# Kernel optimization log

Hardware: AMD Instinct MI355X
Metric: run time of the kernel (lower is better)

Reference implementation:

```python
import jax, jax.numpy as jnp
import numpy as np

S, K, O = 8192, 1024, 4096  # seq_len, in_features, out_features


def setup_inputs() -> dict:
    key = jax.random.key(0)
    k1, k2, k3, k4, k5 = jax.random.split(key, 5)
    x = jax.random.randint(k1, (S, K), -128, 128, dtype=jnp.int8)
    weight_q = jax.random.randint(k2, (O, K), -128, 128, dtype=jnp.int8)
    scale_x = jax.random.uniform(k3, (), jnp.float32, 0.01, 0.1)
    scale_w = jax.random.uniform(k4, (), jnp.float32, 0.01, 0.1)
    scale_y = jax.random.uniform(k5, (S,), jnp.float32, 0.5, 2.0)  # per-row output scale
    return {"x": x, "weight_q": weight_q, "scale_x": scale_x,
            "scale_w": scale_w, "scale_y": scale_y}


def reference(x, weight_q, scale_x, scale_w, scale_y):
    # int8 GEMM with int32 accumulation: [S,K] @ [O,K]^T -> [S,O]
    acc = jnp.einsum('sk,ok->so', x.astype(jnp.int32), weight_q.astype(jnp.int32))
    # fused per-row requantization: scale_y[:seq_len] gives per-row scale
    requant_scale = (scale_x * scale_w / scale_y).astype(jnp.float32)  # [S]
    scaled = acc.astype(jnp.float32) * requant_scale[:, None]
    out_q = jnp.clip(jnp.round(scaled), -128.0, 127.0).astype(jnp.int8)
    return out_q, scale_y
```

## Files before the change

### kernel.cpp

```cpp
#include <hip/hip_runtime.h>


#define S_DIM 8192
#define K_DIM 1024
#define O_DIM 4096
#define BM 128
#define BN 128
#define BK 64
#define NITER (K_DIM / BK)
#define TILE_BYTES (BM * BK)

using i32x4 = __attribute__((ext_vector_type(4))) int;

__device__ __forceinline__ void load_lds16(const void* g, void* l) {
  __builtin_amdgcn_global_load_lds(
      (const __attribute__((address_space(1))) void*)g,
      (__attribute__((address_space(3))) void*)l, 16, 0, 0);
}

__global__ void pack_kernel(const int* __restrict__ xi, const int* __restrict__ wi,
                            const float* __restrict__ sy,
                            uint4* __restrict__ ap, uint4* __restrict__ bp,
                            float* __restrict__ out_sy) {
  const int tid = blockIdx.x * blockDim.x + threadIdx.x;
  const int nA = S_DIM * K_DIM / 16;
  const int nB = O_DIM * K_DIM / 16;

  const int4* s4 = nullptr;
  uint4* dst = nullptr;
  int j = 0;
  if (tid < nA) {
    j = tid;
    const int t = j >> 9, idx = j & 511;
    const int sub = idx >> 6, q = (idx >> 4) & 3, fr = idx & 15;
    const int band = t >> 4, kt = t & 15;
    const int row = band * 128 + sub * 16 + fr;
    s4 = (const int4*)xi + row * 256 + kt * 16 + q * 4;
    dst = ap;
  } else if (tid < nA + nB) {
    j = tid - nA;
    const int t = j >> 9, idx = j & 511;
    const int r = idx >> 2, cs = idx & 3, c = cs ^ (r & 3);
    const int band = t >> 4, kt = t & 15;
    const int row = band * 128 + r;
    s4 = (const int4*)wi + row * 256 + kt * 16 + c * 4;
    dst = bp;
  }
  if (s4) {
    int4 v0 = s4[0], v1 = s4[1], v2 = s4[2], v3 = s4[3];
    uint4 o;
    o.x = (v0.x & 0xff) | ((v0.y & 0xff) << 8) | ((v0.z & 0xff) << 16) | (((unsigned)v0.w & 0xff) << 24);
    o.y = (v1.x & 0xff) | ((v1.y & 0xff) << 8) | ((v1.z & 0xff) << 16) | (((unsigned)v1.w & 0xff) << 24);
    o.z = (v2.x & 0xff) | ((v2.y & 0xff) << 8) | ((v2.z & 0xff) << 16) | (((unsigned)v2.w & 0xff) << 24);
    o.w = (v3.x & 0xff) | ((v3.y & 0xff) << 8) | ((v3.z & 0xff) << 16) | (((unsigned)v3.w & 0xff) << 24);
    dst[j] = o;
  }
  if (tid < S_DIM) out_sy[tid] = sy[tid];
}

__global__ __launch_bounds__(256, 4) void gemm_i8_kernel(
    const signed char* __restrict__ Ap,
    const signed char* __restrict__ Bp,
    const float* __restrict__ sx, const float* __restrict__ sw,
    const float* __restrict__ sy, float* __restrict__ out) {
  __shared__ __align__(16) signed char Bs[2][TILE_BYTES];

  const int tid = threadIdx.x;
  const int wave = tid >> 6;
  const int lane = tid & 63;
  const int wm = wave >> 1;
  const int wn = wave & 1;
  const int rowBase = blockIdx.x * BM;
  const int colBase = blockIdx.y * BN;

  const int soff = wave * 1024 + lane * 16;
  const signed char* gB = Bp + (size_t)blockIdx.y * NITER * TILE_BYTES + soff;
  signed char* ldsB = (signed char*)Bs + wave * 1024;

  const signed char* gA = Ap + (size_t)blockIdx.x * NITER * TILE_BYTES +
                          wm * 4096 + lane * 16;

  i32x4 acc[4][4] = {};

  const int fr = lane & 15;
  const int fq = (((lane >> 4) ^ (fr & 3)) & 3) * 16;

  load_lds16(gB, ldsB);
  load_lds16(gB + 4096, ldsB + 4096);
  i32x4 af[2][4];
#pragma unroll
  for (int mi = 0; mi < 4; ++mi)
    af[0][mi] = *(const i32x4*)(gA + mi * 1024);

  for (int it = 0; it < NITER; ++it) {
    const int p = it & 1;
    __syncthreads();

    if (it + 1 < NITER) {
      const int boff = ((it + 1) & 1) * TILE_BYTES;
      const size_t goff = (size_t)(it + 1) * TILE_BYTES;
      load_lds16(gB + goff, ldsB + boff);
      load_lds16(gB + goff + 4096, ldsB + boff + 4096);
#pragma unroll
      for (int mi = 0; mi < 4; ++mi)
        af[p ^ 1][mi] = *(const i32x4*)(gA + goff + mi * 1024);
    }

    const signed char* curB = Bs[it & 1];
#pragma unroll
    for (int ni = 0; ni < 4; ++ni) {
      i32x4 bf = *(const i32x4*)(curB + (wn * 64 + ni * 16 + fr) * BK + fq);
#pragma unroll
      for (int mi = 0; mi < 4; ++mi)
        acc[mi][ni] =
            __builtin_amdgcn_mfma_i32_16x16x64_i8(af[p][mi], bf, acc[mi][ni], 0, 0, 0);
    }
  }

  const float sxw = sx[0] * sw[0];
  const int quad = lane >> 4;
#pragma unroll
  for (int mi = 0; mi < 4; ++mi) {
#pragma unroll
    for (int r = 0; r < 4; ++r) {
      const int s = rowBase + wm * 64 + mi * 16 + quad * 4 + r;
      const float rs = sxw / sy[s];
      float* orow = out + (size_t)s * O_DIM + colBase + wn * 64 + fr;
#pragma unroll
      for (int ni = 0; ni < 4; ++ni) {
        float f = rintf((float)acc[mi][ni][r] * rs);
        f = fminf(127.0f, fmaxf(-128.0f, f));
        orow[ni * 16] = f;
      }
    }
  }
}

extern "C" void kernel_launch(void* const* d_in, const int* in_sizes, int n_in,
                              void* d_out, int out_size, void* d_ws, size_t ws_size,
                              hipStream_t stream) {
  const int* x = (const int*)d_in[0];
  const int* w = (const int*)d_in[1];
  const float* sx = (const float*)d_in[2];
  const float* sw = (const float*)d_in[3];
  const float* sy = (const float*)d_in[4];
  float* out = (float*)d_out;

  uint4* ap = (uint4*)d_ws;
  uint4* bp = ap + (size_t)S_DIM * K_DIM / 16;

  const int total = S_DIM * K_DIM / 16 + O_DIM * K_DIM / 16;
  pack_kernel<<<(total + 255) / 256, 256, 0, stream>>>(
      x, w, sy, ap, bp, out + (size_t)S_DIM * O_DIM);

  dim3 grid(S_DIM / BM, O_DIM / BN);
  gemm_i8_kernel<<<grid, 256, 0, stream>>>(
      (const signed char*)ap, (const signed char*)bp, sx, sw, sy, out);
}
```

Before: 201.1 us.

## Load B fragments directly from global into registers, dropping LDS and barriers

Result: no change. 204.5 us (+1.7%).

```diff
diff --git a/kernel.cpp b/kernel.cpp
--- a/kernel.cpp
+++ b/kernel.cpp
@@ -12,12 +12,6 @@
 
 using i32x4 = __attribute__((ext_vector_type(4))) int;
 
-__device__ __forceinline__ void load_lds16(const void* g, void* l) {
-  __builtin_amdgcn_global_load_lds(
-      (const __attribute__((address_space(1))) void*)g,
-      (__attribute__((address_space(3))) void*)l, 16, 0, 0);
-}
-
 __global__ void pack_kernel(const int* __restrict__ xi, const int* __restrict__ wi,
                             const float* __restrict__ sy,
                             uint4* __restrict__ ap, uint4* __restrict__ bp,
@@ -26,27 +20,20 @@
   const int nA = S_DIM * K_DIM / 16;
   const int nB = O_DIM * K_DIM / 16;
 
-  const int4* s4 = nullptr;
+  const int4* src = nullptr;
   uint4* dst = nullptr;
   int j = 0;
   if (tid < nA) {
-    j = tid;
+    j = tid; src = (const int4*)xi; dst = ap;
+  } else if (tid < nA + nB) {
+    j = tid - nA; src = (const int4*)wi; dst = bp;
+  }
+  if (dst) {
     const int t = j >> 9, idx = j & 511;
     const int sub = idx >> 6, q = (idx >> 4) & 3, fr = idx & 15;
     const int band = t >> 4, kt = t & 15;
     const int row = band * 128 + sub * 16 + fr;
-    s4 = (const int4*)xi + row * 256 + kt * 16 + q * 4;
-    dst = ap;
-  } else if (tid < nA + nB) {
-    j = tid - nA;
-    const int t = j >> 9, idx = j & 511;
-    const int r = idx >> 2, cs = idx & 3, c = cs ^ (r & 3);
-    const int band = t >> 4, kt = t & 15;
-    const int row = band * 128 + r;
-    s4 = (const int4*)wi + row * 256 + kt * 16 + c * 4;
-    dst = bp;
-  }
-  if (s4) {
+    const int4* s4 = src + row * 256 + kt * 16 + q * 4;
     int4 v0 = s4[0], v1 = s4[1], v2 = s4[2], v3 = s4[3];
     uint4 o;
     o.x = (v0.x & 0xff) | ((v0.y & 0xff) << 8) | ((v0.z & 0xff) << 16) | (((unsigned)v0.w & 0xff) << 24);
@@ -58,13 +45,11 @@
   if (tid < S_DIM) out_sy[tid] = sy[tid];
 }
 
-__global__ __launch_bounds__(256, 4) void gemm_i8_kernel(
+__global__ __launch_bounds__(256, 3) void gemm_i8_kernel(
     const signed char* __restrict__ Ap,
     const signed char* __restrict__ Bp,
     const float* __restrict__ sx, const float* __restrict__ sw,
     const float* __restrict__ sy, float* __restrict__ out) {
-  __shared__ __align__(16) signed char Bs[2][TILE_BYTES];
-
   const int tid = threadIdx.x;
   const int wave = tid >> 6;
   const int lane = tid & 63;
@@ -73,51 +58,41 @@
   const int rowBase = blockIdx.x * BM;
   const int colBase = blockIdx.y * BN;
 
-  const int soff = wave * 1024 + lane * 16;
-  const signed char* gB = Bp + (size_t)blockIdx.y * NITER * TILE_BYTES + soff;
-  signed char* ldsB = (signed char*)Bs + wave * 1024;
-
   const signed char* gA = Ap + (size_t)blockIdx.x * NITER * TILE_BYTES +
                           wm * 4096 + lane * 16;
+  const signed char* gB = Bp + (size_t)blockIdx.y * NITER * TILE_BYTES +
+                          wn * 4096 + lane * 16;
 
   i32x4 acc[4][4] = {};
+  i32x4 af[2][4], bf[2][4];
 
-  const int fr = lane & 15;
-  const int fq = (((lane >> 4) ^ (fr & 3)) & 3) * 16;
+#pragma unroll
+  for (int mi = 0; mi < 4; ++mi) {
+    af[0][mi] = *(const i32x4*)(gA + mi * 1024);
+    bf[0][mi] = *(const i32x4*)(gB + mi * 1024);
+  }
 
-  load_lds16(gB, ldsB);
-  load_lds16(gB + 4096, ldsB + 4096);
-  i32x4 af[2][4];
-#pragma unroll
-  for (int mi = 0; mi < 4; ++mi)
-    af[0][mi] = *(const i32x4*)(gA + mi * 1024);
-
+#pragma unroll 2
   for (int it = 0; it < NITER; ++it) {
     const int p = it & 1;
-    __syncthreads();
-
     if (it + 1 < NITER) {
-      const int boff = ((it + 1) & 1) * TILE_BYTES;
       const size_t goff = (size_t)(it + 1) * TILE_BYTES;
-      load_lds16(gB + goff, ldsB + boff);
-      load_lds16(gB + goff + 4096, ldsB + boff + 4096);
 #pragma unroll
-      for (int mi = 0; mi < 4; ++mi)
+      for (int mi = 0; mi < 4; ++mi) {
         af[p ^ 1][mi] = *(const i32x4*)(gA + goff + mi * 1024);
+        bf[p ^ 1][mi] = *(const i32x4*)(gB + goff + mi * 1024);
+      }
     }
-
-    const signed char* curB = Bs[it & 1];
 #pragma unroll
-    for (int ni = 0; ni < 4; ++ni) {
-      i32x4 bf = *(const i32x4*)(curB + (wn * 64 + ni * 16 + fr) * BK + fq);
+    for (int mi = 0; mi < 4; ++mi)
 #pragma unroll
-      for (int mi = 0; mi < 4; ++mi)
-        acc[mi][ni] =
-            __builtin_amdgcn_mfma_i32_16x16x64_i8(af[p][mi], bf, acc[mi][ni], 0, 0, 0);
-    }
+      for (int ni = 0; ni < 4; ++ni)
+        acc[mi][ni] = __builtin_amdgcn_mfma_i32_16x16x64_i8(
+            af[p][mi], bf[p][ni], acc[mi][ni], 0, 0, 0);
   }
 
   const float sxw = sx[0] * sw[0];
+  const int fr = lane & 15;
   const int quad = lane >> 4;
 #pragma unroll
   for (int mi = 0; mi < 4; ++mi) {
```
